# Performance work log

Measured on AMD Instinct MI355X. Metric: run time of the kernel, lower is better.

Reference implementation:

```python
import jax, jax.numpy as jnp
import numpy as np

N_NODES = 100000
N_EDGES = 1600000
D_IN = 64
D_OUT = 64


def setup_inputs() -> dict:
    key = jax.random.key(0)
    k1, k2, k3, k4 = jax.random.split(key, 4)
    x = jax.random.normal(k1, (N_NODES, D_IN), dtype=jnp.float32)
    src = jax.random.randint(k2, (N_EDGES,), 0, N_NODES, dtype=jnp.int32)
    dst = jax.random.randint(k3, (N_EDGES,), 0, N_NODES, dtype=jnp.int32)
    W = jax.random.normal(k4, (D_OUT, D_IN), dtype=jnp.float32) / np.sqrt(D_IN)
    b = jnp.zeros((D_OUT,), dtype=jnp.float32)
    return {"x": x, "src": src, "dst": dst, "W": W, "b": b}


def reference(x, src, dst, W, b):
    # DGL SAGEConv with 'gcn' aggregator:
    #   h_neigh = (sum_{j in N_in(i)} x_j + x_i) / (in_degree(i) + 1)
    #   out     = h_neigh @ W^T + b
    N = x.shape[0]
    # gather source features and scatter-add into destination nodes  [N, D_IN]
    neigh_sum = jax.ops.segment_sum(x[src], dst, num_segments=N)
    deg = jax.ops.segment_sum(jnp.ones_like(dst, dtype=x.dtype), dst, num_segments=N)
    h_neigh = (neigh_sum + x) / (deg + 1.0)[:, None]
    return h_neigh @ W.T + b
```

## Files before the change

### kernel.cpp

```cpp
#include <hip/hip_runtime.h>

#define D 64
#define BSH 6
#define BSZ 64
#define NBMAX 2048
#define TILE 8192
#define CAP  1536
#define SRTC 2056

typedef unsigned int   uint;
typedef unsigned short ushort_t;
typedef __attribute__((ext_vector_type(8))) short bf16x8;
typedef __attribute__((ext_vector_type(4))) float f32x4;

__device__ __forceinline__ ushort_t f2bf(float f) {
    uint u = __float_as_uint(f);
    u += 0x7FFFu + ((u >> 16) & 1u);
    return (ushort_t)(u >> 16);
}

__global__ __launch_bounds__(256) void k_bhist(
    const int* __restrict__ dst, int* __restrict__ bucketCount,
    int* __restrict__ blockBase, const float4* __restrict__ x4,
    uint4* __restrict__ xb4, int n8, int nb, int n_edges)
{
    __shared__ int hist[NBMAX];
    const int tid = threadIdx.x;
    for (int i = tid; i < nb; i += 256) hist[i] = 0;
    __syncthreads();

    if (blockIdx.x == 0 && tid < 8) {
        uint4 z; z.x = z.y = z.z = z.w = 0u;
        xb4[n8 + tid] = z;
    }

    {
        const int chunk = (n8 + gridDim.x - 1) / gridDim.x;
        const int lo = blockIdx.x * chunk;
        const int hi = min(n8, lo + chunk);
        for (int t = lo + tid; t < hi; t += 256) {
            float4 a = x4[t * 2];
            float4 c = x4[t * 2 + 1];
            uint4 o;
            o.x = (uint)f2bf(a.x) | ((uint)f2bf(a.y) << 16);
            o.y = (uint)f2bf(a.z) | ((uint)f2bf(a.w) << 16);
            o.z = (uint)f2bf(c.x) | ((uint)f2bf(c.y) << 16);
            o.w = (uint)f2bf(c.z) | ((uint)f2bf(c.w) << 16);
            xb4[t] = o;
        }
    }

    const int e0 = blockIdx.x * TILE;
    const int n4 = n_edges >> 2;
    const int4* dst4 = (const int4*)dst;
#pragma unroll
    for (int k = 0; k < TILE / 1024; ++k) {
        int i4 = (e0 >> 2) + k * 256 + tid;
        if (i4 < n4) {
            int4 d = dst4[i4];
            atomicAdd(&hist[d.x >> BSH], 1);
            atomicAdd(&hist[d.y >> BSH], 1);
            atomicAdd(&hist[d.z >> BSH], 1);
            atomicAdd(&hist[d.w >> BSH], 1);
        }
    }
    if (blockIdx.x == gridDim.x - 1) {
        for (int e = (n4 << 2) + tid; e < n_edges; e += 256)
            atomicAdd(&hist[dst[e] >> BSH], 1);
    }
    __syncthreads();
    for (int i = tid; i < nb; i += 256)
        blockBase[(size_t)blockIdx.x * nb + i] = atomicAdd(&bucketCount[i], hist[i]);
}

__global__ __launch_bounds__(256) void k_bscatter(
    const int* __restrict__ src, const int* __restrict__ dst,
    const int* __restrict__ bucketCount, const int* __restrict__ blockBase,
    int* __restrict__ bucketBase, int* __restrict__ packed,
    int nb, int n_edges)
{
    __shared__ int sc[NBMAX];
    __shared__ int cur[NBMAX];
    __shared__ int ts[256];
    const int tid = threadIdx.x;
    const int blk = blockIdx.x;

    {
        const int base = tid * 8;
        int v[8];
#pragma unroll
        for (int k = 0; k < 8; ++k)
            v[k] = (base + k < nb) ? bucketCount[base + k] : 0;
        int tsum = 0;
#pragma unroll
        for (int k = 0; k < 8; ++k) tsum += v[k];
        ts[tid] = tsum;
        __syncthreads();
        for (int off = 1; off < 256; off <<= 1) {
            int t = (tid >= off) ? ts[tid - off] : 0;
            __syncthreads();
            ts[tid] += t;
            __syncthreads();
        }
        int run = ts[tid] - tsum;
#pragma unroll
        for (int k = 0; k < 8; ++k) {
            if (base + k < nb) sc[base + k] = run;
            run += v[k];
        }
    }
    __syncthreads();

    if (blk == 0) {
        for (int i = tid; i <= nb; i += 256)
            bucketBase[i] = (i < nb) ? sc[i] : n_edges;
    }

    for (int i = tid; i < nb; i += 256)
        cur[i] = sc[i] + blockBase[(size_t)blk * nb + i];
    __syncthreads();

    const int e0 = blk * TILE;
    const int n4 = n_edges >> 2;
    const int4* src4 = (const int4*)src;
    const int4* dst4 = (const int4*)dst;
#pragma unroll
    for (int k = 0; k < TILE / 1024; ++k) {
        int i4 = (e0 >> 2) + k * 256 + tid;
        if (i4 < n4) {
            int4 sv = src4[i4];
            int4 dv = dst4[i4];
            int p;
            p = atomicAdd(&cur[dv.x >> BSH], 1); packed[p] = sv.x | ((dv.x & (BSZ-1)) << 24);
            p = atomicAdd(&cur[dv.y >> BSH], 1); packed[p] = sv.y | ((dv.y & (BSZ-1)) << 24);
            p = atomicAdd(&cur[dv.z >> BSH], 1); packed[p] = sv.z | ((dv.z & (BSZ-1)) << 24);
            p = atomicAdd(&cur[dv.w >> BSH], 1); packed[p] = sv.w | ((dv.w & (BSZ-1)) << 24);
        }
    }
    if (blk == gridDim.x - 1) {
        for (int e = (n4 << 2) + tid; e < n_edges; e += 256) {
            int p = atomicAdd(&cur[dst[e] >> BSH], 1);
            packed[p] = src[e] | ((dst[e] & (BSZ-1)) << 24);
        }
    }
}

__global__ __launch_bounds__(512, 8) void k_aggcsr(
    const int* __restrict__ packed, const int* __restrict__ bucketBase,
    const uint4* __restrict__ xb4, const float* __restrict__ W,
    const float* __restrict__ bvec, float* __restrict__ out, int n_nodes)
{
    __shared__ int raw[CAP];
    __shared__ int srt[SRTC];
    __shared__ ushort_t Wl[64 * 64];
    __shared__ int ldeg[BSZ];
    __shared__ int lofs[BSZ];
    __shared__ int cur[BSZ];

    const int tid = threadIdx.x;
    const int bucket = blockIdx.x;
    const int ebase = bucketBase[bucket];
    const int ecnt  = bucketBase[bucket + 1] - ebase;
    const bool fits = (ecnt <= CAP);
    const uint nmax = (uint)(n_nodes - 1);
    const int zrow = n_nodes;

    {
        const int o = tid >> 3;
        const int j = (tid & 7) * 8;
        const float* wp = W + o * 64 + j;
        float4 wa = *(const float4*)wp;
        float4 wb = *(const float4*)(wp + 4);
        uint4 w4;
        w4.x = (uint)f2bf(wa.x) | ((uint)f2bf(wa.y) << 16);
        w4.y = (uint)f2bf(wa.z) | ((uint)f2bf(wa.w) << 16);
        w4.z = (uint)f2bf(wb.x) | ((uint)f2bf(wb.y) << 16);
        w4.w = (uint)f2bf(wb.z) | ((uint)f2bf(wb.w) << 16);
        *(uint4*)((char*)Wl + o * 128 + ((j * 2) ^ ((o & 7) << 4))) = w4;
    }
    if (tid < BSZ) ldeg[tid] = 0;
    __syncthreads();

    if (fits) {
        for (int i = tid; i < ecnt; i += 512) {
            int pk = packed[ebase + i];
            raw[i] = pk;
            atomicAdd(&ldeg[((uint)pk) >> 24], 1);
        }
    } else {
        for (int i = tid; i < ecnt; i += 512)
            atomicAdd(&ldeg[((uint)packed[ebase + i]) >> 24], 1);
    }
    __syncthreads();

    {
        int v = 0;
        if (tid < BSZ) { v = (ldeg[tid] + 3) & ~3; lofs[tid] = v; }
        __syncthreads();
        for (int off = 1; off < BSZ; off <<= 1) {
            int t = (tid < BSZ && tid >= off) ? lofs[tid - off] : 0;
            __syncthreads();
            if (tid < BSZ) lofs[tid] += t;
            __syncthreads();
        }
        if (tid < BSZ) { int e = lofs[tid] - v; lofs[tid] = e; cur[tid] = e; }
    }
    __syncthreads();

    if (fits) {
        for (int i = tid; i < ecnt; i += 512) {
            int pk = raw[i];
            int pos = atomicAdd(&cur[((uint)pk) >> 24], 1);
            srt[pos] = pk & 0x00FFFFFF;
        }
        if (tid < BSZ) {
            int base = lofs[tid] + ldeg[tid];
            int end  = lofs[tid] + ((ldeg[tid] + 3) & ~3);
            for (int i = base; i < end; ++i) srt[i] = zrow;
        }
    }
    __syncthreads();

    const int wave = tid >> 6;
    const int lane = tid & 63;
    const int g    = lane >> 3;
    const int f8   = lane & 7;

#define CVLO(u) __uint_as_float((u) << 16)
#define CVHI(u) __uint_as_float((u) & 0xFFFF0000u)

    const uint4* __restrict__ xbf = xb4 + f8;

    const int nl = wave * 8 + g;
    const int node = (bucket << BSH) + nl;
    const bool valid = (node < n_nodes);
    const int cnt = valid ? ldeg[nl] : 0;
    const int eb  = valid ? lofs[nl] : 0;
    const int pc  = (cnt + 3) & ~3;

    float s0 = 0.f, s1 = 0.f, s2 = 0.f, s3 = 0.f;
    float s4 = 0.f, s5 = 0.f, s6 = 0.f, s7 = 0.f;

    if (fits) {
        for (int i = 0; i < pc; i += 4) {
            uint vv[4];
#pragma unroll
            for (int k = 0; k < 4; ++k) vv[k] = (uint)srt[eb + i + k];
            uint4 A[4];
#pragma unroll
            for (int k = 0; k < 4; ++k)
                A[k] = xbf[(size_t)vv[k] * 8];
#pragma unroll
            for (int k = 0; k < 4; ++k) {
                s0 += CVLO(A[k].x);
                s1 += CVHI(A[k].x);
                s2 += CVLO(A[k].y);
                s3 += CVHI(A[k].y);
                s4 += CVLO(A[k].z);
                s5 += CVHI(A[k].z);
                s6 += CVLO(A[k].w);
                s7 += CVHI(A[k].w);
            }
        }
    } else {
        const int nlm = valid ? nl : -1;
        for (int i = 0; i < ecnt; ++i) {
            int pk = packed[ebase + i];
            float m0 = ((int)(((uint)pk) >> 24) == nlm) ? 1.0f : 0.0f;
            uint4 A0 = xbf[(size_t)min((uint)(pk & 0x00FFFFFF), nmax) * 8];
            s0 = fmaf(m0, CVLO(A0.x), s0);
            s1 = fmaf(m0, CVHI(A0.x), s1);
            s2 = fmaf(m0, CVLO(A0.y), s2);
            s3 = fmaf(m0, CVHI(A0.y), s3);
            s4 = fmaf(m0, CVLO(A0.z), s4);
            s5 = fmaf(m0, CVHI(A0.z), s5);
            s6 = fmaf(m0, CVLO(A0.w), s6);
            s7 = fmaf(m0, CVHI(A0.w), s7);
        }
    }

    uint4 hreg; hreg.x = hreg.y = hreg.z = hreg.w = 0u;
    if (valid) {
        uint4 xv = xbf[(size_t)node * 8];
        float rinv = 1.0f / (float)(cnt + 1);
        float h0 = (s0 + CVLO(xv.x)) * rinv;
        float h1 = (s1 + CVHI(xv.x)) * rinv;
        float h2 = (s2 + CVLO(xv.y)) * rinv;
        float h3 = (s3 + CVHI(xv.y)) * rinv;
        float h4 = (s4 + CVLO(xv.z)) * rinv;
        float h5 = (s5 + CVHI(xv.z)) * rinv;
        float h6 = (s6 + CVLO(xv.w)) * rinv;
        float h7 = (s7 + CVHI(xv.w)) * rinv;
        hreg.x = (uint)f2bf(h0) | ((uint)f2bf(h1) << 16);
        hreg.y = (uint)f2bf(h2) | ((uint)f2bf(h3) << 16);
        hreg.z = (uint)f2bf(h4) | ((uint)f2bf(h5) << 16);
        hreg.w = (uint)f2bf(h6) | ((uint)f2bf(h7) << 16);
    }
#undef CVLO
#undef CVHI

    __syncthreads();

    char* hstage = (char*)srt;
    *(uint4*)(hstage + nl * 128 + ((f8 * 16) ^ ((nl & 7) << 4))) = hreg;
    __syncthreads();

    if (wave < 4) {
        char* hwb = hstage + wave * 2048;
        const int m  = lane & 15;
        const int kg = lane >> 4;
        bf16x8 a0 = *(const bf16x8*)(hwb + m * 128 + (((kg * 16)     ) ^ ((m & 7) << 4)));
        bf16x8 a1 = *(const bf16x8*)(hwb + m * 128 + (((64 + kg * 16)) ^ ((m & 7) << 4)));

        const int node0 = (bucket << BSH) + wave * 16;
#pragma unroll
        for (int c = 0; c < 4; ++c) {
            const int o = c * 16 + m;
            bf16x8 b0 = *(const bf16x8*)((char*)Wl + o * 128 + (((kg * 16)     ) ^ ((o & 7) << 4)));
            bf16x8 b1 = *(const bf16x8*)((char*)Wl + o * 128 + (((64 + kg * 16)) ^ ((o & 7) << 4)));
            f32x4 acc = {0.f, 0.f, 0.f, 0.f};
            acc = __builtin_amdgcn_mfma_f32_16x16x32_bf16(a0, b0, acc, 0, 0, 0);
            acc = __builtin_amdgcn_mfma_f32_16x16x32_bf16(a1, b1, acc, 0, 0, 0);
            const float bias = bvec[o];
#pragma unroll
            for (int r = 0; r < 4; ++r) {
                int row = node0 + kg * 4 + r;
                if (row < n_nodes)
                    out[(size_t)row * 64 + o] = acc[r] + bias;
            }
        }
    }
}

extern "C" void kernel_launch(void* const* d_in, const int* in_sizes, int n_in,
                              void* d_out, int out_size, void* d_ws, size_t ws_size,
                              hipStream_t stream)
{
    const float* x   = (const float*)d_in[0];
    const int*   src = (const int*)d_in[1];
    const int*   dst = (const int*)d_in[2];
    const float* W   = (const float*)d_in[3];
    const float* b   = (const float*)d_in[4];
    float* out = (float*)d_out;

    const int n_nodes = in_sizes[0] / D;
    const int n_edges = in_sizes[1];
    const int nb  = (n_nodes + BSZ - 1) >> BSH;
    const int nbA = (n_edges + TILE - 1) / TILE;

    ushort_t* xb = (ushort_t*)d_ws;
    int* bucketCount = (int*)(xb + (size_t)(n_nodes + 1) * D);
    int* bucketBase  = bucketCount + NBMAX;
    int* blockBase   = bucketBase + NBMAX + 1;
    int* packed      = blockBase + (size_t)nbA * nb;

    hipMemsetAsync(bucketCount, 0, NBMAX * sizeof(int), stream);

    const int n8 = n_nodes * D / 8;
    k_bhist   <<<nbA, 256, 0, stream>>>(dst, bucketCount, blockBase,
                                        (const float4*)x, (uint4*)xb, n8, nb, n_edges);
    k_bscatter<<<nbA, 256, 0, stream>>>(src, dst, bucketCount, blockBase,
                                        bucketBase, packed, nb, n_edges);
    k_aggcsr  <<<nb,  512, 0, stream>>>(packed, bucketBase, (const uint4*)xb,
                                        W, b, out, n_nodes);
}
```

Before: 78.22 us.

## Sort bucket edges by source range per node and widen conversion grid

In the aggregation kernel, each bucket's edges are now sorted by a composite key of source-range tile (src>>15) and local destination node, so each node's neighbour gathers are grouped by source region. The aim is better L2 locality across waves when fetching bf16 feature rows. The histogram kernel is also launched with more blocks so the fp32-to-bf16 conversion of x spreads over more CUs, with the extra blocks exiting before the histogram work. In exchange, the local scan grows from 64 to 256 keys, each key is padded to a multiple of four, and every node loops over four segments.

```diff
diff --git a/kernel.cpp b/kernel.cpp
--- a/kernel.cpp
+++ b/kernel.cpp
@@ -6,7 +6,10 @@
 #define NBMAX 2048
 #define TILE 8192
 #define CAP  1536
-#define SRTC 2056
+#define TSH  15
+#define NT   4
+#define KEYS (BSZ * NT)
+#define SRTC (CAP + KEYS * 3 + 8)
 
 typedef unsigned int   uint;
 typedef unsigned short ushort_t;
@@ -22,21 +25,26 @@
 __global__ __launch_bounds__(256) void k_bhist(
     const int* __restrict__ dst, int* __restrict__ bucketCount,
     int* __restrict__ blockBase, const float4* __restrict__ x4,
-    uint4* __restrict__ xb4, int n8, int nb, int n_edges)
+    uint4* __restrict__ xb4, int n8, int nb, int nbA, int n_edges)
 {
     __shared__ int hist[NBMAX];
     const int tid = threadIdx.x;
-    for (int i = tid; i < nb; i += 256) hist[i] = 0;
-    __syncthreads();
-
-    if (blockIdx.x == 0 && tid < 8) {
+    const int blk = blockIdx.x;
+    const bool doHist = (blk < nbA);
+
+    if (doHist) {
+        for (int i = tid; i < nb; i += 256) hist[i] = 0;
+    }
+    __syncthreads();
+
+    if (blk == 0 && tid < 8) {
         uint4 z; z.x = z.y = z.z = z.w = 0u;
         xb4[n8 + tid] = z;
     }
 
     {
         const int chunk = (n8 + gridDim.x - 1) / gridDim.x;
-        const int lo = blockIdx.x * chunk;
+        const int lo = blk * chunk;
         const int hi = min(n8, lo + chunk);
         for (int t = lo + tid; t < hi; t += 256) {
             float4 a = x4[t * 2];
@@ -50,7 +58,9 @@
         }
     }
 
-    const int e0 = blockIdx.x * TILE;
+    if (!doHist) return;
+
+    const int e0 = blk * TILE;
     const int n4 = n_edges >> 2;
     const int4* dst4 = (const int4*)dst;
 #pragma unroll
@@ -64,13 +74,13 @@
             atomicAdd(&hist[d.w >> BSH], 1);
         }
     }
-    if (blockIdx.x == gridDim.x - 1) {
+    if (blk == nbA - 1) {
         for (int e = (n4 << 2) + tid; e < n_edges; e += 256)
             atomicAdd(&hist[dst[e] >> BSH], 1);
     }
     __syncthreads();
     for (int i = tid; i < nb; i += 256)
-        blockBase[(size_t)blockIdx.x * nb + i] = atomicAdd(&bucketCount[i], hist[i]);
+        blockBase[(size_t)blk * nb + i] = atomicAdd(&bucketCount[i], hist[i]);
 }
 
 __global__ __launch_bounds__(256) void k_bscatter(
@@ -153,9 +163,9 @@
     __shared__ int raw[CAP];
     __shared__ int srt[SRTC];
     __shared__ ushort_t Wl[64 * 64];
-    __shared__ int ldeg[BSZ];
-    __shared__ int lofs[BSZ];
-    __shared__ int cur[BSZ];
+    __shared__ int ldeg[KEYS];
+    __shared__ int lofs[KEYS];
+    __shared__ int cur[KEYS];
 
     const int tid = threadIdx.x;
     const int bucket = blockIdx.x;
@@ -178,42 +188,47 @@
         w4.w = (uint)f2bf(wb.z) | ((uint)f2bf(wb.w) << 16);
         *(uint4*)((char*)Wl + o * 128 + ((j * 2) ^ ((o & 7) << 4))) = w4;
     }
-    if (tid < BSZ) ldeg[tid] = 0;
+    if (tid < KEYS) ldeg[tid] = 0;
     __syncthreads();
 
     if (fits) {
         for (int i = tid; i < ecnt; i += 512) {
             int pk = packed[ebase + i];
             raw[i] = pk;
-            atomicAdd(&ldeg[((uint)pk) >> 24], 1);
+            int key = (((pk & 0x00FFFFFF) >> TSH) << BSH) | (((uint)pk) >> 24);
+            atomicAdd(&ldeg[key], 1);
         }
     } else {
-        for (int i = tid; i < ecnt; i += 512)
-            atomicAdd(&ldeg[((uint)packed[ebase + i]) >> 24], 1);
+        for (int i = tid; i < ecnt; i += 512) {
+            int pk = packed[ebase + i];
+            int key = (((pk & 0x00FFFFFF) >> TSH) << BSH) | (((uint)pk) >> 24);
+            atomicAdd(&ldeg[key], 1);
+        }
     }
     __syncthreads();
 
     {
         int v = 0;
-        if (tid < BSZ) { v = (ldeg[tid] + 3) & ~3; lofs[tid] = v; }
+        if (tid < KEYS) { v = (ldeg[tid] + 3) & ~3; lofs[tid] = v; }
         __syncthreads();
-        for (int off = 1; off < BSZ; off <<= 1) {
-            int t = (tid < BSZ && tid >= off) ? lofs[tid - off] : 0;
+        for (int off = 1; off < KEYS; off <<= 1) {
+            int t = (tid < KEYS && tid >= off) ? lofs[tid - off] : 0;
             __syncthreads();
-            if (tid < BSZ) lofs[tid] += t;
+            if (tid < KEYS) lofs[tid] += t;
             __syncthreads();
         }
-        if (tid < BSZ) { int e = lofs[tid] - v; lofs[tid] = e; cur[tid] = e; }
+        if (tid < KEYS) { int e = lofs[tid] - v; lofs[tid] = e; cur[tid] = e; }
     }
     __syncthreads();
 
     if (fits) {
         for (int i = tid; i < ecnt; i += 512) {
             int pk = raw[i];
-            int pos = atomicAdd(&cur[((uint)pk) >> 24], 1);
+            int key = (((pk & 0x00FFFFFF) >> TSH) << BSH) | (((uint)pk) >> 24);
+            int pos = atomicAdd(&cur[key], 1);
             srt[pos] = pk & 0x00FFFFFF;
         }
-        if (tid < BSZ) {
+        if (tid < KEYS) {
             int base = lofs[tid] + ldeg[tid];
             int end  = lofs[tid] + ((ldeg[tid] + 3) & ~3);
             for (int i = base; i < end; ++i) srt[i] = zrow;
@@ -234,32 +249,38 @@
     const int nl = wave * 8 + g;
     const int node = (bucket << BSH) + nl;
     const bool valid = (node < n_nodes);
-    const int cnt = valid ? ldeg[nl] : 0;
-    const int eb  = valid ? lofs[nl] : 0;
-    const int pc  = (cnt + 3) & ~3;
+
+    int cnt = 0;
+#pragma unroll
+    for (int t = 0; t < NT; ++t) cnt += ldeg[(t << BSH) | nl];
 
     float s0 = 0.f, s1 = 0.f, s2 = 0.f, s3 = 0.f;
     float s4 = 0.f, s5 = 0.f, s6 = 0.f, s7 = 0.f;
 
     if (fits) {
-        for (int i = 0; i < pc; i += 4) {
-            uint vv[4];
-#pragma unroll
-            for (int k = 0; k < 4; ++k) vv[k] = (uint)srt[eb + i + k];
-            uint4 A[4];
-#pragma unroll
-            for (int k = 0; k < 4; ++k)
-                A[k] = xbf[(size_t)vv[k] * 8];
-#pragma unroll
-            for (int k = 0; k < 4; ++k) {
-                s0 += CVLO(A[k].x);
-                s1 += CVHI(A[k].x);
-                s2 += CVLO(A[k].y);
-                s3 += CVHI(A[k].y);
-                s4 += CVLO(A[k].z);
-                s5 += CVHI(A[k].z);
-                s6 += CVLO(A[k].w);
-                s7 += CVHI(A[k].w);
+        for (int t = 0; t < NT; ++t) {
+            const int key = (t << BSH) | nl;
+            const int eb = lofs[key];
+            const int pcnt = (ldeg[key] + 3) & ~3;
+            for (int i = 0; i < pcnt; i += 4) {
+                uint vv[4];
+#pragma unroll
+                for (int k = 0; k < 4; ++k) vv[k] = (uint)srt[eb + i + k];
+                uint4 A[4];
+#pragma unroll
+                for (int k = 0; k < 4; ++k)
+                    A[k] = xbf[(size_t)vv[k] * 8];
+#pragma unroll
+                for (int k = 0; k < 4; ++k) {
+                    s0 += CVLO(A[k].x);
+                    s1 += CVHI(A[k].x);
+                    s2 += CVLO(A[k].y);
+                    s3 += CVHI(A[k].y);
+                    s4 += CVLO(A[k].z);
+                    s5 += CVHI(A[k].z);
+                    s6 += CVLO(A[k].w);
+                    s7 += CVHI(A[k].w);
+                }
             }
         }
     } else {
@@ -357,8 +378,10 @@
     hipMemsetAsync(bucketCount, 0, NBMAX * sizeof(int), stream);
 
     const int n8 = n_nodes * D / 8;
-    k_bhist   <<<nbA, 256, 0, stream>>>(dst, bucketCount, blockBase,
-                                        (const float4*)x, (uint4*)xb, n8, nb, n_edges);
+    const int nbConv = (n8 + 1023) / 1024;
+    const int gridA = max(nbA, nbConv);
+    k_bhist   <<<gridA, 256, 0, stream>>>(dst, bucketCount, blockBase,
+                                          (const float4*)x, (uint4*)xb, n8, nb, nbA, n_edges);
     k_bscatter<<<nbA, 256, 0, stream>>>(src, dst, bucketCount, blockBase,
                                         bucketBase, packed, nb, n_edges);
     k_aggcsr  <<<nb,  512, 0, stream>>>(packed, bucketBase, (const uint4*)xb,
```

Measured after the change: 79.30 us. About the same (+1.4%).

## Split bucket sort from gather/GEMM kernel and widen x conversion grid

Applied to the files above, without the earlier changes.

The fused aggregate kernel is split in two. A sort kernel writes per-bucket CSR (padded source lists plus per-node offsets and degrees) to global memory, and a lighter gather kernel uses 256 threads and a 4 KB staging buffer with no sort LDS, which should allow higher occupancy during the latency-bound gather. The x-to-bf16 conversion grid is also enlarged beyond the histogram block count so the conversion is spread over more blocks. The cost is an extra kernel launch and an extra global write and read of the sorted edge list. The old masked fallback path for oversized buckets is replaced by a global scatter.

```diff
diff --git a/kernel.cpp b/kernel.cpp
--- a/kernel.cpp
+++ b/kernel.cpp
@@ -6,7 +6,8 @@
 #define NBMAX 2048
 #define TILE 8192
 #define CAP  1536
-#define SRTC 2056
+#define PADM (BSZ * 3)
+#define SRTC (CAP + PADM + 8)
 
 typedef unsigned int   uint;
 typedef unsigned short ushort_t;
@@ -22,21 +23,26 @@
 __global__ __launch_bounds__(256) void k_bhist(
     const int* __restrict__ dst, int* __restrict__ bucketCount,
     int* __restrict__ blockBase, const float4* __restrict__ x4,
-    uint4* __restrict__ xb4, int n8, int nb, int n_edges)
+    uint4* __restrict__ xb4, int n8, int nb, int nbA, int n_edges)
 {
     __shared__ int hist[NBMAX];
     const int tid = threadIdx.x;
-    for (int i = tid; i < nb; i += 256) hist[i] = 0;
-    __syncthreads();
-
-    if (blockIdx.x == 0 && tid < 8) {
+    const int blk = blockIdx.x;
+    const bool doHist = (blk < nbA);
+
+    if (doHist) {
+        for (int i = tid; i < nb; i += 256) hist[i] = 0;
+    }
+    __syncthreads();
+
+    if (blk == 0 && tid < 8) {
         uint4 z; z.x = z.y = z.z = z.w = 0u;
         xb4[n8 + tid] = z;
     }
 
     {
         const int chunk = (n8 + gridDim.x - 1) / gridDim.x;
-        const int lo = blockIdx.x * chunk;
+        const int lo = blk * chunk;
         const int hi = min(n8, lo + chunk);
         for (int t = lo + tid; t < hi; t += 256) {
             float4 a = x4[t * 2];
@@ -50,7 +56,9 @@
         }
     }
 
-    const int e0 = blockIdx.x * TILE;
+    if (!doHist) return;
+
+    const int e0 = blk * TILE;
     const int n4 = n_edges >> 2;
     const int4* dst4 = (const int4*)dst;
 #pragma unroll
@@ -64,13 +72,13 @@
             atomicAdd(&hist[d.w >> BSH], 1);
         }
     }
-    if (blockIdx.x == gridDim.x - 1) {
+    if (blk == nbA - 1) {
         for (int e = (n4 << 2) + tid; e < n_edges; e += 256)
             atomicAdd(&hist[dst[e] >> BSH], 1);
     }
     __syncthreads();
     for (int i = tid; i < nb; i += 256)
-        blockBase[(size_t)blockIdx.x * nb + i] = atomicAdd(&bucketCount[i], hist[i]);
+        blockBase[(size_t)blk * nb + i] = atomicAdd(&bucketCount[i], hist[i]);
 }
 
 __global__ __launch_bounds__(256) void k_bscatter(
@@ -145,14 +153,13 @@
     }
 }
 
-__global__ __launch_bounds__(512, 8) void k_aggcsr(
+__global__ __launch_bounds__(256) void k_sort(
     const int* __restrict__ packed, const int* __restrict__ bucketBase,
-    const uint4* __restrict__ xb4, const float* __restrict__ W,
-    const float* __restrict__ bvec, float* __restrict__ out, int n_nodes)
+    int* __restrict__ esrcP, int* __restrict__ pofs, int* __restrict__ pdeg,
+    int n_nodes)
 {
     __shared__ int raw[CAP];
     __shared__ int srt[SRTC];
-    __shared__ ushort_t Wl[64 * 64];
     __shared__ int ldeg[BSZ];
     __shared__ int lofs[BSZ];
     __shared__ int cur[BSZ];
@@ -161,13 +168,88 @@
     const int bucket = blockIdx.x;
     const int ebase = bucketBase[bucket];
     const int ecnt  = bucketBase[bucket + 1] - ebase;
+    const int gbase = ebase + PADM * bucket;
     const bool fits = (ecnt <= CAP);
-    const uint nmax = (uint)(n_nodes - 1);
     const int zrow = n_nodes;
 
+    if (tid < BSZ) ldeg[tid] = 0;
+    __syncthreads();
+
+    if (fits) {
+        for (int i = tid; i < ecnt; i += 256) {
+            int pk = packed[ebase + i];
+            raw[i] = pk;
+            atomicAdd(&ldeg[((uint)pk) >> 24], 1);
+        }
+    } else {
+        for (int i = tid; i < ecnt; i += 256)
+            atomicAdd(&ldeg[((uint)packed[ebase + i]) >> 24], 1);
+    }
+    __syncthreads();
+
     {
-        const int o = tid >> 3;
-        const int j = (tid & 7) * 8;
+        int v = 0;
+        if (tid < BSZ) { v = (ldeg[tid] + 3) & ~3; lofs[tid] = v; }
+        __syncthreads();
+        for (int off = 1; off < BSZ; off <<= 1) {
+            int t = (tid < BSZ && tid >= off) ? lofs[tid - off] : 0;
+            __syncthreads();
+            if (tid < BSZ) lofs[tid] += t;
+            __syncthreads();
+        }
+        if (tid < BSZ) { int e = lofs[tid] - v; lofs[tid] = e; cur[tid] = e; }
+    }
+    __syncthreads();
+
+    if (fits) {
+        for (int i = tid; i < ecnt; i += 256) {
+            int pk = raw[i];
+            int pos = atomicAdd(&cur[((uint)pk) >> 24], 1);
+            srt[pos] = pk & 0x00FFFFFF;
+        }
+        if (tid < BSZ) {
+            int base = lofs[tid] + ldeg[tid];
+            int end  = lofs[tid] + ((ldeg[tid] + 3) & ~3);
+            for (int i = base; i < end; ++i) srt[i] = zrow;
+        }
+        __syncthreads();
+        const int ptot = lofs[BSZ - 1] + ((ldeg[BSZ - 1] + 3) & ~3);
+        for (int i = tid; i < ptot; i += 256) esrcP[gbase + i] = srt[i];
+    } else {
+        for (int i = tid; i < ecnt; i += 256) {
+            int pk = packed[ebase + i];
+            int pos = atomicAdd(&cur[((uint)pk) >> 24], 1);
+            esrcP[gbase + pos] = pk & 0x00FFFFFF;
+        }
+        __syncthreads();
+        if (tid < BSZ) {
+            int base = lofs[tid] + ldeg[tid];
+            int end  = lofs[tid] + ((ldeg[tid] + 3) & ~3);
+            for (int i = base; i < end; ++i) esrcP[gbase + i] = zrow;
+        }
+    }
+
+    if (tid < BSZ) {
+        int node = (bucket << BSH) + tid;
+        pofs[node] = gbase + lofs[tid];
+        pdeg[node] = ldeg[tid];
+    }
+}
+
+__global__ __launch_bounds__(256, 8) void k_gather(
+    const int* __restrict__ esrcP, const int* __restrict__ pofs,
+    const int* __restrict__ pdeg, const uint4* __restrict__ xb4,
+    const float* __restrict__ W, const float* __restrict__ bvec,
+    float* __restrict__ out, int n_nodes)
+{
+    __shared__ ushort_t Wl[64 * 64];
+    __shared__ __align__(16) char hst[4][2048];
+
+    const int tid = threadIdx.x;
+
+    for (int item = tid; item < 512; item += 256) {
+        const int o = item >> 3;
+        const int j = (item & 7) * 8;
         const float* wp = W + o * 64 + j;
         float4 wa = *(const float4*)wp;
         float4 wb = *(const float4*)(wp + 4);
@@ -178,47 +260,6 @@
         w4.w = (uint)f2bf(wb.z) | ((uint)f2bf(wb.w) << 16);
         *(uint4*)((char*)Wl + o * 128 + ((j * 2) ^ ((o & 7) << 4))) = w4;
     }
-    if (tid < BSZ) ldeg[tid] = 0;
-    __syncthreads();
-
-    if (fits) {
-        for (int i = tid; i < ecnt; i += 512) {
-            int pk = packed[ebase + i];
-            raw[i] = pk;
-            atomicAdd(&ldeg[((uint)pk) >> 24], 1);
-        }
-    } else {
-        for (int i = tid; i < ecnt; i += 512)
-            atomicAdd(&ldeg[((uint)packed[ebase + i]) >> 24], 1);
-    }
-    __syncthreads();
-
-    {
-        int v = 0;
-        if (tid < BSZ) { v = (ldeg[tid] + 3) & ~3; lofs[tid] = v; }
-        __syncthreads();
-        for (int off = 1; off < BSZ; off <<= 1) {
-            int t = (tid < BSZ && tid >= off) ? lofs[tid - off] : 0;
-            __syncthreads();
-            if (tid < BSZ) lofs[tid] += t;
-            __syncthreads();
-        }
-        if (tid < BSZ) { int e = lofs[tid] - v; lofs[tid] = e; cur[tid] = e; }
-    }
-    __syncthreads();
-
-    if (fits) {
-        for (int i = tid; i < ecnt; i += 512) {
-            int pk = raw[i];
-            int pos = atomicAdd(&cur[((uint)pk) >> 24], 1);
-            srt[pos] = pk & 0x00FFFFFF;
-        }
-        if (tid < BSZ) {
-            int base = lofs[tid] + ldeg[tid];
-            int end  = lofs[tid] + ((ldeg[tid] + 3) & ~3);
-            for (int i = base; i < end; ++i) srt[i] = zrow;
-        }
-    }
     __syncthreads();
 
     const int wave = tid >> 6;
@@ -230,22 +271,25 @@
 #define CVHI(u) __uint_as_float((u) & 0xFFFF0000u)
 
     const uint4* __restrict__ xbf = xb4 + f8;
-
-    const int nl = wave * 8 + g;
-    const int node = (bucket << BSH) + nl;
-    const bool valid = (node < n_nodes);
-    const int cnt = valid ? ldeg[nl] : 0;
-    const int eb  = valid ? lofs[nl] : 0;
-    const int pc  = (cnt + 3) & ~3;
-
-    float s0 = 0.f, s1 = 0.f, s2 = 0.f, s3 = 0.f;
-    float s4 = 0.f, s5 = 0.f, s6 = 0.f, s7 = 0.f;
-
-    if (fits) {
+    char* hwb = hst[wave];
+    const int tile = blockIdx.x * 4 + wave;
+    const int node0 = tile * 16;
+
+#pragma unroll
+    for (int p = 0; p < 2; ++p) {
+        const int nl = p * 8 + g;
+        const int node = node0 + nl;
+        const int cnt = pdeg[node];
+        const int eb  = pofs[node];
+        const int pc  = (cnt + 3) & ~3;
+
+        float s0 = 0.f, s1 = 0.f, s2 = 0.f, s3 = 0.f;
+        float s4 = 0.f, s5 = 0.f, s6 = 0.f, s7 = 0.f;
+
         for (int i = 0; i < pc; i += 4) {
             uint vv[4];
 #pragma unroll
-            for (int k = 0; k < 4; ++k) vv[k] = (uint)srt[eb + i + k];
+            for (int k = 0; k < 4; ++k) vv[k] = (uint)esrcP[eb + i + k];
             uint4 A[4];
 #pragma unroll
             for (int k = 0; k < 4; ++k)
@@ -262,72 +306,48 @@
                 s7 += CVHI(A[k].w);
             }
         }
-    } else {
-        const int nlm = valid ? nl : -1;
-        for (int i = 0; i < ecnt; ++i) {
-            int pk = packed[ebase + i];
-            float m0 = ((int)(((uint)pk) >> 24) == nlm) ? 1.0f : 0.0f;
-            uint4 A0 = xbf[(size_t)min((uint)(pk & 0x00FFFFFF), nmax) * 8];
-            s0 = fmaf(m0, CVLO(A0.x), s0);
-            s1 = fmaf(m0, CVHI(A0.x), s1);
-            s2 = fmaf(m0, CVLO(A0.y), s2);
-            s3 = fmaf(m0, CVHI(A0.y), s3);
-            s4 = fmaf(m0, CVLO(A0.z), s4);
-            s5 = fmaf(m0, CVHI(A0.z), s5);
-            s6 = fmaf(m0, CVLO(A0.w), s6);
-            s7 = fmaf(m0, CVHI(A0.w), s7);
-        }
-    }
-
-    uint4 hreg; hreg.x = hreg.y = hreg.z = hreg.w = 0u;
-    if (valid) {
-        uint4 xv = xbf[(size_t)node * 8];
-        float rinv = 1.0f / (float)(cnt + 1);
-        float h0 = (s0 + CVLO(xv.x)) * rinv;
-        float h1 = (s1 + CVHI(xv.x)) * rinv;
-        float h2 = (s2 + CVLO(xv.y)) * rinv;
-        float h3 = (s3 + CVHI(xv.y)) * rinv;
-        float h4 = (s4 + CVLO(xv.z)) * rinv;
-        float h5 = (s5 + CVHI(xv.z)) * rinv;
-        float h6 = (s6 + CVLO(xv.w)) * rinv;
-        float h7 = (s7 + CVHI(xv.w)) * rinv;
-        hreg.x = (uint)f2bf(h0) | ((uint)f2bf(h1) << 16);
-        hreg.y = (uint)f2bf(h2) | ((uint)f2bf(h3) << 16);
-        hreg.z = (uint)f2bf(h4) | ((uint)f2bf(h5) << 16);
-        hreg.w = (uint)f2bf(h6) | ((uint)f2bf(h7) << 16);
+
+        uint4 hreg; hreg.x = hreg.y = hreg.z = hreg.w = 0u;
+        if (node < n_nodes) {
+            uint4 xv = xbf[(size_t)node * 8];
+            float rinv = 1.0f / (float)(cnt + 1);
+            float h0 = (s0 + CVLO(xv.x)) * rinv;
+            float h1 = (s1 + CVHI(xv.x)) * rinv;
+            float h2 = (s2 + CVLO(xv.y)) * rinv;
+            float h3 = (s3 + CVHI(xv.y)) * rinv;
+            float h4 = (s4 + CVLO(xv.z)) * rinv;
+            float h5 = (s5 + CVHI(xv.z)) * rinv;
+            float h6 = (s6 + CVLO(xv.w)) * rinv;
+            float h7 = (s7 + CVHI(xv.w)) * rinv;
+            hreg.x = (uint)f2bf(h0) | ((uint)f2bf(h1) << 16);
+            hreg.y = (uint)f2bf(h2) | ((uint)f2bf(h3) << 16);
+            hreg.z = (uint)f2bf(h4) | ((uint)f2bf(h5) << 16);
+            hreg.w = (uint)f2bf(h6) | ((uint)f2bf(h7) << 16);
+        }
+        *(uint4*)(hwb + nl * 128 + ((f8 * 16) ^ ((nl & 7) << 4))) = hreg;
     }
 #undef CVLO
 #undef CVHI
 
-    __syncthreads();
-
-    char* hstage = (char*)srt;
-    *(uint4*)(hstage + nl * 128 + ((f8 * 16) ^ ((nl & 7) << 4))) = hreg;
-    __syncthreads();
-
-    if (wave < 4) {
-        char* hwb = hstage + wave * 2048;
-        const int m  = lane & 15;
-        const int kg = lane >> 4;
-        bf16x8 a0 = *(const bf16x8*)(hwb + m * 128 + (((kg * 16)     ) ^ ((m & 7) << 4)));
-        bf16x8 a1 = *(const bf16x8*)(hwb + m * 128 + (((64 + kg * 16)) ^ ((m & 7) << 4)));
-
-        const int node0 = (bucket << BSH) + wave * 16;
-#pragma unroll
-        for (int c = 0; c < 4; ++c) {
-            const int o = c * 16 + m;
-            bf16x8 b0 = *(const bf16x8*)((char*)Wl + o * 128 + (((kg * 16)     ) ^ ((o & 7) << 4)));
-            bf16x8 b1 = *(const bf16x8*)((char*)Wl + o * 128 + (((64 + kg * 16)) ^ ((o & 7) << 4)));
-            f32x4 acc = {0.f, 0.f, 0.f, 0.f};
-            acc = __builtin_amdgcn_mfma_f32_16x16x32_bf16(a0, b0, acc, 0, 0, 0);
-            acc = __builtin_amdgcn_mfma_f32_16x16x32_bf16(a1, b1, acc, 0, 0, 0);
-            const float bias = bvec[o];
-#pragma unroll
-            for (int r = 0; r < 4; ++r) {
-                int row = node0 + kg * 4 + r;
-                if (row < n_nodes)
-                    out[(size_t)row * 64 + o] = acc[r] + bias;
-            }
+    const int m  = lane & 15;
+    const int kg = lane >> 4;
+    bf16x8 a0 = *(const bf16x8*)(hwb + m * 128 + (((kg * 16)     ) ^ ((m & 7) << 4)));
+    bf16x8 a1 = *(const bf16x8*)(hwb + m * 128 + (((64 + kg * 16)) ^ ((m & 7) << 4)));
+
+#pragma unroll
+    for (int c = 0; c < 4; ++c) {
+        const int o = c * 16 + m;
+        bf16x8 b0 = *(const bf16x8*)((char*)Wl + o * 128 + (((kg * 16)     ) ^ ((o & 7) << 4)));
+        bf16x8 b1 = *(const bf16x8*)((char*)Wl + o * 128 + (((64 + kg * 16)) ^ ((o & 7) << 4)));
+        f32x4 acc = {0.f, 0.f, 0.f, 0.f};
+        acc = __builtin_amdgcn_mfma_f32_16x16x32_bf16(a0, b0, acc, 0, 0, 0);
+        acc = __builtin_amdgcn_mfma_f32_16x16x32_bf16(a1, b1, acc, 0, 0, 0);
+        const float bias = bvec[o];
+#pragma unroll
+        for (int r = 0; r < 4; ++r) {
+            int row = node0 + kg * 4 + r;
+            if (row < n_nodes)
+                out[(size_t)row * 64 + o] = acc[r] + bias;
         }
     }
 }
@@ -353,14 +373,20 @@
     int* bucketBase  = bucketCount + NBMAX;
     int* blockBase   = bucketBase + NBMAX + 1;
     int* packed      = blockBase + (size_t)nbA * nb;
+    int* esrcP       = packed + n_edges;
+    int* pofs        = esrcP + n_edges + (size_t)PADM * nb;
+    int* pdeg        = pofs + (size_t)nb * BSZ;
 
     hipMemsetAsync(bucketCount, 0, NBMAX * sizeof(int), stream);
 
     const int n8 = n_nodes * D / 8;
-    k_bhist   <<<nbA, 256, 0, stream>>>(dst, bucketCount, blockBase,
-                                        (const float4*)x, (uint4*)xb, n8, nb, n_edges);
+    const int nbConv = (n8 + 1023) / 1024;
+    const int gridA = max(nbA, nbConv);
+    k_bhist   <<<gridA, 256, 0, stream>>>(dst, bucketCount, blockBase,
+                                          (const float4*)x, (uint4*)xb, n8, nb, nbA, n_edges);
     k_bscatter<<<nbA, 256, 0, stream>>>(src, dst, bucketCount, blockBase,
                                         bucketBase, packed, nb, n_edges);
-    k_aggcsr  <<<nb,  512, 0, stream>>>(packed, bucketBase, (const uint4*)xb,
+    k_sort    <<<nb,  256, 0, stream>>>(packed, bucketBase, esrcP, pofs, pdeg, n_nodes);
+    k_gather  <<<nb,  256, 0, stream>>>(esrcP, pofs, pdeg, (const uint4*)xb,
                                         W, b, out, n_nodes);
 }
```

Measured after the change: 83.39 us. 1.07x slower.
